# Optimization experiments

Measured on AMD Instinct MI355X. Metric: run time of the kernel, lower is better.

The kernel has to match this reference:

```python
import jax, jax.numpy as jnp
import numpy as np

NL, DM, DS, DC, EX = 4, 1024, 16, 4, 2
DI = EX * DM          # 2048 inner dim
DTR = DM // 16        # 64 dt_rank
HID, OUT = 2048, 1000
B, L = 2, 1024
EPS = 1e-5

def _ln(x, w, b):
    m = jnp.mean(x, -1, keepdims=True)
    v = jnp.var(x, -1, keepdims=True)
    return (x - m) / jnp.sqrt(v + EPS) * w + b

def _silu(x):
    return x * jax.nn.sigmoid(x)

def _dwconv(x, w, b):
    # x: (B,L,C), w: (C,K) depthwise causal conv
    K = w.shape[1]
    xp = jnp.pad(x, ((0, 0), (K - 1, 0), (0, 0)))
    kern = jnp.transpose(w)[:, None, :]  # (K,1,C)
    y = jax.lax.conv_general_dilated(xp, kern, (1,), 'VALID',
                                     dimension_numbers=('NLC', 'LIO', 'NLC'),
                                     feature_group_count=x.shape[-1])
    return y + b

def _selective_scan(xs_, dt, Bm, Cm, A, Dv):
    # xs_, dt: (B,L,DI); Bm, Cm: (B,L,DS); A: (DI,DS); Dv: (DI,)
    def step(h, inp):
        x_t, dt_t, B_t, C_t = inp  # (B,DI),(B,DI),(B,DS),(B,DS)
        dA = jnp.exp(dt_t[..., None] * A)                       # (B,DI,DS)
        h = dA * h + dt_t[..., None] * B_t[:, None, :] * x_t[..., None]
        return h, jnp.einsum('bdn,bn->bd', h, C_t)
    h0 = jnp.zeros((xs_.shape[0], A.shape[0], A.shape[1]), xs_.dtype)
    seq = tuple(jnp.swapaxes(t, 0, 1) for t in (xs_, dt, Bm, Cm))
    _, ys = jax.lax.scan(step, h0, seq)
    return jnp.swapaxes(ys, 0, 1) + xs_ * Dv

def _mamba_block(x, ipw, cw, cb, xpw, dpw, dpb, Alog, Dv, opw):
    xz = jnp.einsum('bld,ed->ble', x, ipw)          # (B,L,2*DI)
    xs_, z = jnp.split(xz, 2, -1)
    xs_ = _silu(_dwconv(xs_, cw, cb))
    xdbl = jnp.einsum('bld,ed->ble', xs_, xpw)      # (B,L,DTR+2*DS)
    dt, Bm, Cm = jnp.split(xdbl, [DTR, DTR + DS], -1)
    dt = jax.nn.softplus(jnp.einsum('blr,dr->bld', dt, dpw) + dpb)
    A = -jnp.exp(Alog)
    y = _selective_scan(xs_, dt, Bm, Cm, A, Dv)
    y = y * _silu(z)
    return jnp.einsum('bld,ed->ble', y, opw)

def setup_inputs() -> dict:
    key = jax.random.key(0)
    ks = jax.random.split(key, 16)
    s = 0.02
    return {
        'x': jax.random.normal(ks[0], (B, L, DM), jnp.float32),
        'ln_w': jnp.ones((NL, DM)), 'ln_b': jnp.zeros((NL, DM)),
        'in_proj_w': jax.random.normal(ks[1], (NL, 2 * DI, DM)) * s,
        'conv_w': jax.random.normal(ks[2], (NL, DI, DC)) * s,
        'conv_b': jnp.zeros((NL, DI)),
        'x_proj_w': jax.random.normal(ks[3], (NL, DTR + 2 * DS, DI)) * s,
        'dt_proj_w': jax.random.normal(ks[4], (NL, DI, DTR)) * s,
        'dt_proj_b': jax.random.uniform(ks[5], (NL, DI), minval=-4.0, maxval=-2.0),
        'A_log': jnp.log(jnp.broadcast_to(jnp.arange(1, DS + 1, dtype=jnp.float32), (NL, DI, DS)) + 0.0),
        'Dv': jnp.ones((NL, DI)),
        'out_proj_w': jax.random.normal(ks[6], (NL, DM, DI)) * s,
        'fn_w': jnp.ones((DM,)), 'fn_b': jnp.zeros((DM,)),
        'h1_w': jax.random.normal(ks[7], (HID, DM)) * s, 'h1_b': jnp.zeros((HID,)),
        'hln_w': jnp.ones((HID,)), 'hln_b': jnp.zeros((HID,)),
        'h2_w': jax.random.normal(ks[8], (OUT, HID)) * s, 'h2_b': jnp.zeros((OUT,)),
    }

def reference(x, ln_w, ln_b, in_proj_w, conv_w, conv_b, x_proj_w, dt_proj_w,
              dt_proj_b, A_log, Dv, out_proj_w, fn_w, fn_b,
              h1_w, h1_b, hln_w, hln_b, h2_w, h2_b):
    for i in range(NL):
        res = x
        xn = _ln(x, ln_w[i], ln_b[i])
        x = _mamba_block(xn, in_proj_w[i], conv_w[i], conv_b[i], x_proj_w[i],
                         dt_proj_w[i], dt_proj_b[i], A_log[i], Dv[i], out_proj_w[i]) + res
    x = _ln(x, fn_w, fn_b)
    last = x[:, -1, :]                               # (B, DM)
    h = jax.nn.gelu(_ln(last @ h1_w.T + h1_b, hln_w, hln_b), approximate=False)
    return h @ h2_w.T + h2_b                         # (B, OUT)
```

## Files before the change

kernel.cpp:

```cpp
#include <hip/hip_runtime.h>

typedef unsigned short u16;
using short8 = __attribute__((ext_vector_type(8))) short;
using f32x4  = __attribute__((ext_vector_type(4))) float;

#define NLAYER 4
#define DMODEL 1024
#define DSTATE 16
#define DINNER 2048
#define DTRANK 64
#define SEQL   1024
#define NBATCH 2
#define MTOK   2048
#define NCH    64
#define CLEN   16

__device__ __forceinline__ u16 f2bf(float f) {
  union { float f; unsigned int u; } cv; cv.f = f;
  return (u16)((cv.u + 0x7FFFu + ((cv.u >> 16) & 1u)) >> 16);
}
__device__ __forceinline__ float bf2f(u16 v) {
  union { unsigned int u; float f; } cv; cv.u = ((unsigned int)v) << 16; return cv.f;
}

__global__ __launch_bounds__(256) void f32_to_bf16_l(const float* __restrict__ src,
                                                     u16* __restrict__ dst, int nper) {
  int l = blockIdx.y;
  int i4 = (blockIdx.x * 256 + threadIdx.x) * 4;
  if (i4 >= nper) return;
  float4 v = *(const float4*)&src[(size_t)l * nper + i4];
  ushort4 o; o.x = f2bf(v.x); o.y = f2bf(v.y); o.z = f2bf(v.z); o.w = f2bf(v.w);
  *(ushort4*)&dst[(size_t)l * nper + i4] = o;
}

__global__ __launch_bounds__(256) void cvt_pad_xproj_l(const float* __restrict__ src,
                                                       u16* __restrict__ dst) {
  int l = blockIdx.y;
  int i4 = (blockIdx.x * 256 + threadIdx.x) * 4;
  int row = i4 >> 11, col = i4 & 2047;
  float4 v = make_float4(0.f, 0.f, 0.f, 0.f);
  if (row < 96) v = *(const float4*)&src[(size_t)l * 96 * 2048 + row * 2048 + col];
  ushort4 o; o.x = f2bf(v.x); o.y = f2bf(v.y); o.z = f2bf(v.z); o.w = f2bf(v.w);
  *(ushort4*)&dst[(size_t)l * 128 * 2048 + i4] = o;
}

__global__ __launch_bounds__(256) void ln_to_bf16_k(const float* __restrict__ X,
    const float* __restrict__ w, const float* __restrict__ b, u16* __restrict__ out) {
  int row = blockIdx.x, tid = threadIdx.x;
  const float* x = X + (size_t)row * 1024;
  float4 v = ((const float4*)x)[tid];
  float s = v.x + v.y + v.z + v.w;
  float q = v.x*v.x + v.y*v.y + v.z*v.z + v.w*v.w;
  for (int o = 32; o; o >>= 1) { s += __shfl_down(s, o); q += __shfl_down(q, o); }
  __shared__ float sb[4], qb[4];
  int wv = tid >> 6, lane = tid & 63;
  if (lane == 0) { sb[wv] = s; qb[wv] = q; }
  __syncthreads();
  s = sb[0] + sb[1] + sb[2] + sb[3];
  q = qb[0] + qb[1] + qb[2] + qb[3];
  float mean = s * (1.f / 1024.f);
  float var  = q * (1.f / 1024.f) - mean * mean;
  float rstd = rsqrtf(var + 1e-5f);
  float4 wv4 = ((const float4*)w)[tid];
  float4 bv4 = ((const float4*)b)[tid];
  ushort4 o4;
  o4.x = f2bf((v.x - mean) * rstd * wv4.x + bv4.x);
  o4.y = f2bf((v.y - mean) * rstd * wv4.y + bv4.y);
  o4.z = f2bf((v.z - mean) * rstd * wv4.z + bv4.z);
  o4.w = f2bf((v.w - mean) * rstd * wv4.w + bv4.w);
  ((ushort4*)(out + (size_t)row * 1024))[tid] = o4;
}

__device__ __forceinline__ void stage_tile(const u16* G, int ld, int row0, int k0,
                                           u16* S, int tid) {
  int w = tid >> 6;
#pragma unroll
  for (int j = 0; j < 2; ++j) {
    int t = tid + j * 256;
    int r = t >> 2;
    int c = (t & 3) << 3;
    const u16* g = G + (size_t)(row0 + r) * ld + (k0 + c);
    u16* s = S + w * 512 + j * 2048;
    __builtin_amdgcn_global_load_lds((const __attribute__((address_space(1))) void*)g,
                                     (__attribute__((address_space(3))) void*)s,
                                     16, 0, 0);
  }
}

template<int EPI, int SWZ>
__global__ __launch_bounds__(256) void gemm_bt(const u16* __restrict__ A,
    const u16* __restrict__ Bw, float* __restrict__ C,
    int lda, int ldb, int ldc, int kchunk, int nbm) {
  __shared__ u16 As[2][128 * 32];
  __shared__ u16 Bs[2][128 * 32];
  int tid = threadIdx.x;
  int bm, bn;
  if (SWZ) {
    int l = blockIdx.x;
    int xcd = l & 7;
    int idx = l >> 3;
    int bnr = (int)(gridDim.x >> 3) / nbm;
    bm = idx % nbm;
    bn = xcd * bnr + idx / nbm;
  } else {
    bm = blockIdx.x; bn = blockIdx.y;
  }
  int kb = blockIdx.z * kchunk, ke = kb + kchunk;
  int lane = tid & 63, w = tid >> 6;
  int wr = (w >> 1) * 64, wc = (w & 1) * 64;
  int fr = lane & 15;
  int kg = (lane >> 4) * 8;
  f32x4 acc[4][4] = {};
  int cur = 0;
  stage_tile(A, lda, bm * 128, kb, As[0], tid);
  stage_tile(Bw, ldb, bn * 128, kb, Bs[0], tid);
  __syncthreads();
  for (int k0 = kb; k0 < ke; k0 += 32) {
    int kn = k0 + 32;
    if (kn < ke) {
      stage_tile(A, lda, bm * 128, kn, As[cur ^ 1], tid);
      stage_tile(Bw, ldb, bn * 128, kn, Bs[cur ^ 1], tid);
    }
    short8 a[4], b[4];
#pragma unroll
    for (int mf = 0; mf < 4; ++mf)
      a[mf] = *(const short8*)&As[cur][(wr + mf * 16 + fr) * 32 + kg];
#pragma unroll
    for (int nf = 0; nf < 4; ++nf)
      b[nf] = *(const short8*)&Bs[cur][(wc + nf * 16 + fr) * 32 + kg];
#pragma unroll
    for (int mf = 0; mf < 4; ++mf)
#pragma unroll
      for (int nf = 0; nf < 4; ++nf)
        acc[mf][nf] = __builtin_amdgcn_mfma_f32_16x16x32_bf16(a[mf], b[nf], acc[mf][nf], 0, 0, 0);
    __syncthreads();
    cur ^= 1;
  }
  int r0 = bm * 128 + wr + (lane >> 4) * 4;
  int c0 = bn * 128 + wc + fr;
#pragma unroll
  for (int mf = 0; mf < 4; ++mf) {
#pragma unroll
    for (int nf = 0; nf < 4; ++nf) {
#pragma unroll
      for (int r = 0; r < 4; ++r) {
        int gr = r0 + mf * 16 + r;
        int gc = c0 + nf * 16;
        float v = acc[mf][nf][r];
        size_t idx = (size_t)gr * ldc + gc;
        if (EPI == 1) {
          ((u16*)C)[idx] = f2bf(v);
        } else {
          atomicAdd(&C[idx], v);
        }
      }
    }
  }
}

__global__ __launch_bounds__(256) void conv_silu_k(const u16* __restrict__ xzb,
    const float* __restrict__ cw, const float* __restrict__ cb,
    u16* __restrict__ xsb) {
  int idx = blockIdx.x * 256 + threadIdx.x;
  int m = idx >> 8;
  int d = (idx & 255) << 3;
  int t = m & (SEQL - 1);
  float4 w4[8];
#pragma unroll
  for (int i = 0; i < 8; ++i) w4[i] = *(const float4*)&cw[(d + i) * 4];
  float acc[8];
#pragma unroll
  for (int q = 0; q < 2; ++q) {
    float4 c4 = *(const float4*)&cb[d + q * 4];
    acc[q*4+0] = c4.x; acc[q*4+1] = c4.y; acc[q*4+2] = c4.z; acc[q*4+3] = c4.w;
  }
#pragma unroll
  for (int j = 0; j < 4; ++j) {
    int tt = t - 3 + j;
    if (tt >= 0) {
      short8 xv = *(const short8*)&xzb[(size_t)(m - 3 + j) * 4096 + d];
#pragma unroll
      for (int i = 0; i < 8; ++i)
        acc[i] += bf2f((u16)xv[i]) * ((const float*)&w4[i])[j];
    }
  }
  short8 ob;
#pragma unroll
  for (int i = 0; i < 8; ++i) {
    float o = acc[i] / (1.f + __expf(-acc[i]));
    ob[i] = (short)f2bf(o);
  }
  *(short8*)&xsb[(size_t)m * 2048 + d] = ob;
}

__global__ __launch_bounds__(256) void gemm_dt_k(const float* __restrict__ Af,
    const u16* __restrict__ Bw, const float* __restrict__ bias, u16* __restrict__ Cout) {
  __shared__ u16 As[128 * 32];
  __shared__ u16 Bs[128 * 32];
  int tid = threadIdx.x;
  int bm = blockIdx.x, bn = blockIdx.y;
  int lane = tid & 63, w = tid >> 6;
  int wr = (w >> 1) * 64, wc = (w & 1) * 64;
  int fr = lane & 15;
  int kg = (lane >> 4) * 8;
  f32x4 acc[4][4] = {};
  int r  = tid >> 1;
  int cc = (tid & 1) * 16;
  for (int k0 = 0; k0 < 64; k0 += 32) {
    const float* src = &Af[(size_t)(bm * 128 + r) * 128 + k0 + cc];
    float4 f0 = *(const float4*)&src[0];
    float4 f1 = *(const float4*)&src[4];
    float4 f2 = *(const float4*)&src[8];
    float4 f3 = *(const float4*)&src[12];
    short8 o0, o1;
    o0[0]=(short)f2bf(f0.x); o0[1]=(short)f2bf(f0.y); o0[2]=(short)f2bf(f0.z); o0[3]=(short)f2bf(f0.w);
    o0[4]=(short)f2bf(f1.x); o0[5]=(short)f2bf(f1.y); o0[6]=(short)f2bf(f1.z); o0[7]=(short)f2bf(f1.w);
    o1[0]=(short)f2bf(f2.x); o1[1]=(short)f2bf(f2.y); o1[2]=(short)f2bf(f2.z); o1[3]=(short)f2bf(f2.w);
    o1[4]=(short)f2bf(f3.x); o1[5]=(short)f2bf(f3.y); o1[6]=(short)f2bf(f3.z); o1[7]=(short)f2bf(f3.w);
    __syncthreads();
    *(short8*)&As[r * 32 + cc]     = o0;
    *(short8*)&As[r * 32 + cc + 8] = o1;
    stage_tile(Bw, 64, bn * 128, k0, Bs, tid);
    __syncthreads();
    short8 a[4], b[4];
#pragma unroll
    for (int mf = 0; mf < 4; ++mf)
      a[mf] = *(const short8*)&As[(wr + mf * 16 + fr) * 32 + kg];
#pragma unroll
    for (int nf = 0; nf < 4; ++nf)
      b[nf] = *(const short8*)&Bs[(wc + nf * 16 + fr) * 32 + kg];
#pragma unroll
    for (int mf = 0; mf < 4; ++mf)
#pragma unroll
      for (int nf = 0; nf < 4; ++nf)
        acc[mf][nf] = __builtin_amdgcn_mfma_f32_16x16x32_bf16(a[mf], b[nf], acc[mf][nf], 0, 0, 0);
  }
  int r0 = bm * 128 + wr + (lane >> 4) * 4;
  int c0 = bn * 128 + wc + fr;
#pragma unroll
  for (int mf = 0; mf < 4; ++mf)
#pragma unroll
    for (int nf = 0; nf < 4; ++nf)
#pragma unroll
      for (int rr = 0; rr < 4; ++rr) {
        int gr = r0 + bm * 0 + mf * 16 + rr;
        int gc = c0 + nf * 16;
        float v = acc[mf][nf][rr] + bias[gc];
        v = (v > 20.f) ? v : log1pf(__expf(v));
        Cout[(size_t)gr * 2048 + gc] = f2bf(v);
      }
}

__global__ __launch_bounds__(256) void scan_part1(const u16* __restrict__ dtb,
    const u16* __restrict__ xsb, const float* __restrict__ xdbl,
    const float* __restrict__ Alog, float* __restrict__ PS_S, float* __restrict__ sumdt_a) {
  int tid = threadIdx.x;
  int dg = blockIdx.x & 7;
  int ch = (blockIdx.x >> 3) & (NCH - 1);
  int b  = blockIdx.x >> 9;
  int d  = dg * 256 + tid;
  float Ar[16];
#pragma unroll
  for (int q = 0; q < 4; ++q) {
    float4 a = *(const float4*)&Alog[d * 16 + q * 4];
    Ar[q*4+0] = -__expf(a.x); Ar[q*4+1] = -__expf(a.y);
    Ar[q*4+2] = -__expf(a.z); Ar[q*4+3] = -__expf(a.w);
  }
  __shared__ float Bsh[CLEN][16];
  {
    int t = tid >> 4, n = tid & 15;
    int mm = b * SEQL + ch * CLEN + t;
    Bsh[t][n] = xdbl[mm * 128 + 64 + n];
  }
  __syncthreads();
  int mbase = b * SEQL + ch * CLEN;
  float dtv[CLEN], xv[CLEN];
#pragma unroll
  for (int t = 0; t < CLEN; ++t) dtv[t] = bf2f(dtb[(size_t)(mbase + t) * 2048 + d]);
#pragma unroll
  for (int t = 0; t < CLEN; ++t) xv[t] = bf2f(xsb[(size_t)(mbase + t) * 2048 + d]);
  float S[16];
#pragma unroll
  for (int n = 0; n < 16; ++n) S[n] = 0.f;
  float sumdt = 0.f;
  for (int t = 0; t < CLEN; ++t) {
    sumdt += dtv[t];
    float dx = dtv[t] * xv[t];
    float4 B0 = *(const float4*)&Bsh[t][0];
    float4 B1 = *(const float4*)&Bsh[t][4];
    float4 B2 = *(const float4*)&Bsh[t][8];
    float4 B3 = *(const float4*)&Bsh[t][12];
    const float* Bp[4] = {(const float*)&B0, (const float*)&B1, (const float*)&B2, (const float*)&B3};
#pragma unroll
    for (int n = 0; n < 16; ++n)
      S[n] = __expf(dtv[t] * Ar[n]) * S[n] + dx * Bp[n >> 2][n & 3];
  }
  size_t base = ((size_t)(b * NCH + ch) * 16) * 2048 + d;
#pragma unroll
  for (int n = 0; n < 16; ++n) PS_S[base + (size_t)n * 2048] = S[n];
  sumdt_a[(size_t)(b * NCH + ch) * 2048 + d] = sumdt;
}

__global__ __launch_bounds__(256) void scan_prefix(const float* __restrict__ PS_S,
    const float* __restrict__ sumdt_a, const float* __restrict__ Alog,
    u16* __restrict__ Hb) {
  int id = blockIdx.x * 256 + threadIdx.x;
  int d = id & 2047;
  int n = (id >> 11) & 15;
  int b = id >> 15;
  float Ar = -__expf(Alog[d * 16 + n]);
  size_t sbase = ((size_t)(b * NCH) * 16 + n) * 2048 + d;
  size_t dbase = (size_t)(b * NCH) * 2048 + d;
  float h = 0.f;
#pragma unroll 8
  for (int ch = 0; ch < NCH; ++ch) {
    Hb[sbase + (size_t)ch * (16 * 2048)] = f2bf(h);
    float S  = PS_S[sbase + (size_t)ch * (16 * 2048)];
    float sd = sumdt_a[dbase + (size_t)ch * 2048];
    h = fmaf(__expf(Ar * sd), h, S);
  }
}

__global__ __launch_bounds__(256) void scan_part2(const u16* __restrict__ dtb,
    const u16* __restrict__ xsb, const float* __restrict__ xdbl,
    const float* __restrict__ Alog, const float* __restrict__ Dv,
    const u16* __restrict__ xzb, const u16* __restrict__ Hb,
    u16* __restrict__ yg) {
  int tid = threadIdx.x;
  int dg = blockIdx.x & 7;
  int ch = (blockIdx.x >> 3) & (NCH - 1);
  int b  = blockIdx.x >> 9;
  int d  = dg * 256 + tid;
  float Ar[16];
#pragma unroll
  for (int q = 0; q < 4; ++q) {
    float4 a = *(const float4*)&Alog[d * 16 + q * 4];
    Ar[q*4+0] = -__expf(a.x); Ar[q*4+1] = -__expf(a.y);
    Ar[q*4+2] = -__expf(a.z); Ar[q*4+3] = -__expf(a.w);
  }
  float Dvd = Dv[d];
  __shared__ float BCs[CLEN][32];
  {
    int t = tid >> 5, n = tid & 31;
    int mm = b * SEQL + ch * CLEN + t;
    BCs[t][n] = xdbl[mm * 128 + 64 + n];
    BCs[t + 8][n] = xdbl[(mm + 8) * 128 + 64 + n];
  }
  size_t hbase = ((size_t)(b * NCH + ch) * 16) * 2048 + d;
  float h[16];
#pragma unroll
  for (int n = 0; n < 16; ++n) h[n] = bf2f(Hb[hbase + (size_t)n * 2048]);
  int mbase = b * SEQL + ch * CLEN;
  float dtv[CLEN], xv[CLEN], zv[CLEN];
#pragma unroll
  for (int t = 0; t < CLEN; ++t) dtv[t] = bf2f(dtb[(size_t)(mbase + t) * 2048 + d]);
#pragma unroll
  for (int t = 0; t < CLEN; ++t) xv[t] = bf2f(xsb[(size_t)(mbase + t) * 2048 + d]);
#pragma unroll
  for (int t = 0; t < CLEN; ++t) zv[t] = bf2f(xzb[(size_t)(mbase + t) * 4096 + 2048 + d]);
  __syncthreads();
  for (int t = 0; t < CLEN; ++t) {
    float dx = dtv[t] * xv[t];
    float4 B0 = *(const float4*)&BCs[t][0];
    float4 B1 = *(const float4*)&BCs[t][4];
    float4 B2 = *(const float4*)&BCs[t][8];
    float4 B3 = *(const float4*)&BCs[t][12];
    float4 C0 = *(const float4*)&BCs[t][16];
    float4 C1 = *(const float4*)&BCs[t][20];
    float4 C2 = *(const float4*)&BCs[t][24];
    float4 C3 = *(const float4*)&BCs[t][28];
    const float* Bp[4] = {(const float*)&B0, (const float*)&B1, (const float*)&B2, (const float*)&B3};
    const float* Cp[4] = {(const float*)&C0, (const float*)&C1, (const float*)&C2, (const float*)&C3};
#pragma unroll
    for (int n = 0; n < 16; ++n)
      h[n] = __expf(dtv[t] * Ar[n]) * h[n] + dx * Bp[n >> 2][n & 3];
    float y0 = 0.f, y1 = 0.f, y2 = 0.f, y3 = 0.f;
#pragma unroll
    for (int n = 0; n < 4; ++n) {
      y0 += h[n]      * Cp[0][n];
      y1 += h[4 + n]  * Cp[1][n];
      y2 += h[8 + n]  * Cp[2][n];
      y3 += h[12 + n] * Cp[3][n];
    }
    float y = (y0 + y1) + (y2 + y3) + xv[t] * Dvd;
    float sz = zv[t] / (1.f + __expf(-zv[t]));
    yg[(size_t)(mbase + t) * 2048 + d] = f2bf(y * sz);
  }
}

__global__ __launch_bounds__(256) void lnlast_gemv1_k(const float* __restrict__ xb,
    const float* __restrict__ fnw, const float* __restrict__ fnb,
    const float* __restrict__ h1w, const float* __restrict__ h1b,
    float* __restrict__ hpre) {
  int blk = blockIdx.x, tid = threadIdx.x;
  int b = blk >> 9;
  int jbase = (blk & 511) * 4;
  int wv = tid >> 6, lane = tid & 63;
  const float* x = xb + (size_t)(b * 1024 + 1023) * 1024;
  float4 v = ((const float4*)x)[tid];
  float s = v.x + v.y + v.z + v.w;
  float q = v.x*v.x + v.y*v.y + v.z*v.z + v.w*v.w;
  for (int o = 32; o; o >>= 1) { s += __shfl_down(s, o); q += __shfl_down(q, o); }
  __shared__ float sb[4], qb[4];
  __shared__ float row[1024];
  if (lane == 0) { sb[wv] = s; qb[wv] = q; }
  __syncthreads();
  s = sb[0] + sb[1] + sb[2] + sb[3];
  q = qb[0] + qb[1] + qb[2] + qb[3];
  float mean = s * (1.f / 1024.f);
  float rstd = rsqrtf(q * (1.f / 1024.f) - mean * mean + 1e-5f);
  float4 wv4 = ((const float4*)fnw)[tid];
  float4 bv4 = ((const float4*)fnb)[tid];
  float4 o;
  o.x = (v.x - mean) * rstd * wv4.x + bv4.x;
  o.y = (v.y - mean) * rstd * wv4.y + bv4.y;
  o.z = (v.z - mean) * rstd * wv4.z + bv4.z;
  o.w = (v.w - mean) * rstd * wv4.w + bv4.w;
  ((float4*)row)[tid] = o;
  __syncthreads();
  int j = jbase + wv;
  const float* w = h1w + (size_t)j * 1024;
  float acc = 0.f;
#pragma unroll
  for (int qq = 0; qq < 4; ++qq) {
    int col = qq * 256 + lane * 4;
    float4 xv = *(const float4*)&row[col];
    float4 wvv = *(const float4*)&w[col];
    acc += xv.x*wvv.x + xv.y*wvv.y + xv.z*wvv.z + xv.w*wvv.w;
  }
  for (int o2 = 32; o2; o2 >>= 1) acc += __shfl_down(acc, o2);
  if (lane == 0) hpre[b * 2048 + j] = acc + h1b[j];
}

__global__ __launch_bounds__(256) void lngelu_gemv2_k(const float* __restrict__ hpre,
    const float* __restrict__ hlnw, const float* __restrict__ hlnb,
    const float* __restrict__ h2w, const float* __restrict__ h2b,
    float* __restrict__ out) {
  int blk = blockIdx.x, tid = threadIdx.x;
  int b = (blk >= 250) ? 1 : 0;
  int jbase = (blk - b * 250) * 4;
  int wv = tid >> 6, lane = tid & 63;
  const float* x = hpre + b * 2048;
  float4 v0 = ((const float4*)x)[tid];
  float4 v1 = ((const float4*)x)[tid + 256];
  float s = v0.x+v0.y+v0.z+v0.w + v1.x+v1.y+v1.z+v1.w;
  float q = v0.x*v0.x+v0.y*v0.y+v0.z*v0.z+v0.w*v0.w
          + v1.x*v1.x+v1.y*v1.y+v1.z*v1.z+v1.w*v1.w;
  for (int o = 32; o; o >>= 1) { s += __shfl_down(s, o); q += __shfl_down(q, o); }
  __shared__ float sb[4], qb[4];
  __shared__ float row[2048];
  if (lane == 0) { sb[wv] = s; qb[wv] = q; }
  __syncthreads();
  s = sb[0] + sb[1] + sb[2] + sb[3];
  q = qb[0] + qb[1] + qb[2] + qb[3];
  float mean = s * (1.f / 2048.f);
  float rstd = rsqrtf(q * (1.f / 2048.f) - mean * mean + 1e-5f);
#pragma unroll
  for (int h = 0; h < 2; ++h) {
    float4 v = h ? v1 : v0;
    int c0 = tid * 4 + h * 1024;
    float4 wv4 = *(const float4*)&hlnw[c0];
    float4 bv4 = *(const float4*)&hlnb[c0];
    float4 g;
    g.x = (v.x - mean) * rstd * wv4.x + bv4.x;
    g.y = (v.y - mean) * rstd * wv4.y + bv4.y;
    g.z = (v.z - mean) * rstd * wv4.z + bv4.z;
    g.w = (v.w - mean) * rstd * wv4.w + bv4.w;
    g.x = 0.5f * g.x * (1.f + erff(g.x * 0.70710678f));
    g.y = 0.5f * g.y * (1.f + erff(g.y * 0.70710678f));
    g.z = 0.5f * g.z * (1.f + erff(g.z * 0.70710678f));
    g.w = 0.5f * g.w * (1.f + erff(g.w * 0.70710678f));
    *(float4*)&row[c0] = g;
  }
  __syncthreads();
  int j = jbase + wv;
  const float* w = h2w + (size_t)j * 2048;
  float acc = 0.f;
#pragma unroll
  for (int qq = 0; qq < 8; ++qq) {
    int col = qq * 256 + lane * 4;
    float4 xv = *(const float4*)&row[col];
    float4 wvv = *(const float4*)&w[col];
    acc += xv.x*wvv.x + xv.y*wvv.y + xv.z*wvv.z + xv.w*wvv.w;
  }
  for (int o2 = 32; o2; o2 >>= 1) acc += __shfl_down(acc, o2);
  if (lane == 0) out[b * 1000 + j] = acc + h2b[j];
}

extern "C" void kernel_launch(void* const* d_in, const int* in_sizes, int n_in,
                              void* d_out, int out_size, void* d_ws, size_t ws_size,
                              hipStream_t stream) {
  const float* x_in = (const float*)d_in[0];
  const float* lnw  = (const float*)d_in[1];
  const float* lnb  = (const float*)d_in[2];
  const float* ipw  = (const float*)d_in[3];
  const float* cw   = (const float*)d_in[4];
  const float* cb   = (const float*)d_in[5];
  const float* xpw  = (const float*)d_in[6];
  const float* dpw  = (const float*)d_in[7];
  const float* dpb  = (const float*)d_in[8];
  const float* Alog = (const float*)d_in[9];
  const float* Dv   = (const float*)d_in[10];
  const float* opw  = (const float*)d_in[11];
  const float* fnw  = (const float*)d_in[12];
  const float* fnb  = (const float*)d_in[13];
  const float* h1w  = (const float*)d_in[14];
  const float* h1b  = (const float*)d_in[15];
  const float* hlnw = (const float*)d_in[16];
  const float* hlnb = (const float*)d_in[17];
  const float* h2w  = (const float*)d_in[18];
  const float* h2b  = (const float*)d_in[19];
  float* out = (float*)d_out;

  char* ws = (char*)d_ws;
  size_t off = 0;
  auto alloc = [&](size_t bytes) -> void* {
    void* p = ws + off; off += (bytes + 255) & ~(size_t)255; return p;
  };
  float* x_buf   = (float*)alloc((size_t)MTOK * DMODEL * 4);
  u16*   xn_bf   = (u16*)  alloc((size_t)MTOK * DMODEL * 2);
  u16*   xz_bf   = (u16*)  alloc((size_t)MTOK * 2 * DINNER * 2);
  u16*   xs_bf   = (u16*)  alloc((size_t)MTOK * DINNER * 2);
  float* xdbl4   = (float*)alloc((size_t)NLAYER * MTOK * 128 * 4);
  u16*   dtb     = (u16*)  alloc((size_t)MTOK * DINNER * 2);
  u16*   yg_bf   = (u16*)  alloc((size_t)MTOK * DINNER * 2);
  u16*   w_ip4   = (u16*)  alloc((size_t)NLAYER * 2 * DINNER * DMODEL * 2);
  u16*   w_xp4   = (u16*)  alloc((size_t)NLAYER * 128 * DINNER * 2);
  u16*   w_dt4   = (u16*)  alloc((size_t)NLAYER * DINNER * DTRANK * 2);
  u16*   w_op4   = (u16*)  alloc((size_t)NLAYER * DMODEL * DINNER * 2);
  float* PS_S    = (float*)alloc((size_t)NBATCH * NCH * 16 * 2048 * 4);
  float* sumdt_a = (float*)alloc((size_t)NBATCH * NCH * 2048 * 4);
  u16*   Hb      = (u16*)  alloc((size_t)NBATCH * NCH * 16 * 2048 * 2);
  float* hpre    = (float*)alloc(2 * 2048 * 4);

  hipMemcpyAsync(x_buf, x_in, (size_t)MTOK * DMODEL * 4, hipMemcpyDeviceToDevice, stream);
  { dim3 g(4096, 4); f32_to_bf16_l<<<g, 256, 0, stream>>>(ipw, w_ip4, 2 * DINNER * DMODEL); }
  { dim3 g(256, 4);  cvt_pad_xproj_l<<<g, 256, 0, stream>>>(xpw, w_xp4); }
  { dim3 g(128, 4);  f32_to_bf16_l<<<g, 256, 0, stream>>>(dpw, w_dt4, DINNER * DTRANK); }
  { dim3 g(2048, 4); f32_to_bf16_l<<<g, 256, 0, stream>>>(opw, w_op4, DMODEL * DINNER); }
  hipMemsetAsync(xdbl4, 0, (size_t)NLAYER * MTOK * 128 * 4, stream);

  for (int i = 0; i < NLAYER; ++i) {
    float* xdbl_l = xdbl4 + (size_t)i * MTOK * 128;
    ln_to_bf16_k<<<MTOK, 256, 0, stream>>>(x_buf, lnw + i * DMODEL, lnb + i * DMODEL, xn_bf);
    gemm_bt<1, 1><<<dim3(512, 1, 1), 256, 0, stream>>>(
        xn_bf, w_ip4 + (size_t)i * 2 * DINNER * DMODEL, (float*)xz_bf,
        1024, 1024, 4096, 1024, 16);
    conv_silu_k<<<2048, 256, 0, stream>>>(xz_bf, cw + (size_t)i * DINNER * 4, cb + i * DINNER, xs_bf);
    { dim3 g(16, 1, 16);
      gemm_bt<3, 0><<<g, 256, 0, stream>>>(xs_bf, w_xp4 + (size_t)i * 128 * DINNER,
                                           xdbl_l, 2048, 2048, 128, 128, 16); }
    { dim3 g(16, 16, 1);
      gemm_dt_k<<<g, 256, 0, stream>>>(xdbl_l, w_dt4 + (size_t)i * DINNER * DTRANK,
                                       dpb + i * DINNER, dtb); }
    scan_part1<<<1024, 256, 0, stream>>>(dtb, xs_bf, xdbl_l,
                                         Alog + (size_t)i * DINNER * DSTATE, PS_S, sumdt_a);
    scan_prefix<<<256, 256, 0, stream>>>(PS_S, sumdt_a, Alog + (size_t)i * DINNER * DSTATE, Hb);
    scan_part2<<<1024, 256, 0, stream>>>(dtb, xs_bf, xdbl_l, Alog + (size_t)i * DINNER * DSTATE,
                                         Dv + i * DINNER, xz_bf, Hb, yg_bf);
    gemm_bt<3, 1><<<dim3(128, 1, 2), 256, 0, stream>>>(
        yg_bf, w_op4 + (size_t)i * DMODEL * DINNER, x_buf,
        2048, 2048, 1024, 1024, 16);
  }
  lnlast_gemv1_k<<<1024, 256, 0, stream>>>(x_buf, fnw, fnb, h1w, h1b, hpre);
  lngelu_gemv2_k<<<500, 256, 0, stream>>>(hpre, hlnw, hlnb, h2w, h2b, out);
  (void)in_sizes; (void)n_in; (void)out_size; (void)ws_size;
}
```

Measured before the change: 750.5 us.

## Widen GEMM blocks to 512 threads and replace x_proj atomics with split-K reduce

The bf16 MFMA GEMM now runs 8 waves per 128x128 tile, each computing a 64x32 sub-tile, and one 16-byte LDS-direct load per thread per operand. The aim is more waves per CU for latency hiding and fewer accumulator registers per thread. The x_proj split-K GEMM now writes per-split partial results to a scratch buffer, and a separate kernel sums the 16 partials. This replaces the fp32 atomicAdd traffic and the up-front memset, at the cost of one extra launch and extra global memory traffic for the partials.

```diff
diff --git a/kernel.cpp b/kernel.cpp
--- a/kernel.cpp
+++ b/kernel.cpp
@@ -14,6 +14,7 @@
 #define MTOK   2048
 #define NCH    64
 #define CLEN   16
+#define XPK    16
 
 __device__ __forceinline__ u16 f2bf(float f) {
   union { float f; unsigned int u; } cv; cv.f = f;
@@ -86,11 +87,21 @@
                                      16, 0, 0);
   }
 }
+__device__ __forceinline__ void stage512(const u16* G, int ld, int row0, int k0,
+                                         u16* S, int tid) {
+  int r = tid >> 2;
+  int c = (tid & 3) << 3;
+  const u16* g = G + (size_t)(row0 + r) * ld + (k0 + c);
+  u16* s = S + (tid >> 6) * 512;
+  __builtin_amdgcn_global_load_lds((const __attribute__((address_space(1))) void*)g,
+                                   (__attribute__((address_space(3))) void*)s,
+                                   16, 0, 0);
+}
 
 template<int EPI, int SWZ>
-__global__ __launch_bounds__(256) void gemm_bt(const u16* __restrict__ A,
+__global__ __launch_bounds__(512) void gemm_bt(const u16* __restrict__ A,
     const u16* __restrict__ Bw, float* __restrict__ C,
-    int lda, int ldb, int ldc, int kchunk, int nbm) {
+    int lda, int ldb, int ldc, int kchunk, int nbm, int zstride) {
   __shared__ u16 As[2][128 * 32];
   __shared__ u16 Bs[2][128 * 32];
   int tid = threadIdx.x;
@@ -106,49 +117,54 @@
     bm = blockIdx.x; bn = blockIdx.y;
   }
   int kb = blockIdx.z * kchunk, ke = kb + kchunk;
-  int lane = tid & 63, w = tid >> 6;
-  int wr = (w >> 1) * 64, wc = (w & 1) * 64;
+  int lane = tid & 63;
+  int w = tid >> 6;
+  int wr = (w >> 2) * 64;
+  int wc = (w & 3) * 32;
   int fr = lane & 15;
   int kg = (lane >> 4) * 8;
-  f32x4 acc[4][4] = {};
+  f32x4 acc[4][2] = {};
   int cur = 0;
-  stage_tile(A, lda, bm * 128, kb, As[0], tid);
-  stage_tile(Bw, ldb, bn * 128, kb, Bs[0], tid);
+  stage512(A, lda, bm * 128, kb, As[0], tid);
+  stage512(Bw, ldb, bn * 128, kb, Bs[0], tid);
   __syncthreads();
   for (int k0 = kb; k0 < ke; k0 += 32) {
     int kn = k0 + 32;
     if (kn < ke) {
-      stage_tile(A, lda, bm * 128, kn, As[cur ^ 1], tid);
-      stage_tile(Bw, ldb, bn * 128, kn, Bs[cur ^ 1], tid);
+      stage512(A, lda, bm * 128, kn, As[cur ^ 1], tid);
+      stage512(Bw, ldb, bn * 128, kn, Bs[cur ^ 1], tid);
     }
-    short8 a[4], b[4];
+    short8 a[4], b[2];
 #pragma unroll
     for (int mf = 0; mf < 4; ++mf)
       a[mf] = *(const short8*)&As[cur][(wr + mf * 16 + fr) * 32 + kg];
 #pragma unroll
-    for (int nf = 0; nf < 4; ++nf)
+    for (int nf = 0; nf < 2; ++nf)
       b[nf] = *(const short8*)&Bs[cur][(wc + nf * 16 + fr) * 32 + kg];
 #pragma unroll
     for (int mf = 0; mf < 4; ++mf)
 #pragma unroll
-      for (int nf = 0; nf < 4; ++nf)
+      for (int nf = 0; nf < 2; ++nf)
         acc[mf][nf] = __builtin_amdgcn_mfma_f32_16x16x32_bf16(a[mf], b[nf], acc[mf][nf], 0, 0, 0);
     __syncthreads();
     cur ^= 1;
   }
   int r0 = bm * 128 + wr + (lane >> 4) * 4;
   int c0 = bn * 128 + wc + fr;
+  size_t zoff = (EPI == 0) ? (size_t)blockIdx.z * zstride : 0;
 #pragma unroll
   for (int mf = 0; mf < 4; ++mf) {
 #pragma unroll
-    for (int nf = 0; nf < 4; ++nf) {
+    for (int nf = 0; nf < 2; ++nf) {
 #pragma unroll
       for (int r = 0; r < 4; ++r) {
         int gr = r0 + mf * 16 + r;
         int gc = c0 + nf * 16;
         float v = acc[mf][nf][r];
         size_t idx = (size_t)gr * ldc + gc;
-        if (EPI == 1) {
+        if (EPI == 0) {
+          C[zoff + idx] = v;
+        } else if (EPI == 1) {
           ((u16*)C)[idx] = f2bf(v);
         } else {
           atomicAdd(&C[idx], v);
@@ -156,6 +172,18 @@
       }
     }
   }
+}
+
+__global__ __launch_bounds__(256) void reduce_xdbl_k(const float* __restrict__ part,
+                                                     float* __restrict__ xdbl_l) {
+  int i4 = (blockIdx.x * 256 + threadIdx.x) * 4;
+  float4 s = *(const float4*)&part[i4];
+#pragma unroll
+  for (int z = 1; z < XPK; ++z) {
+    float4 v = *(const float4*)&part[(size_t)z * (MTOK * 128) + i4];
+    s.x += v.x; s.y += v.y; s.z += v.z; s.w += v.w;
+  }
+  *(float4*)&xdbl_l[i4] = s;
 }
 
 __global__ __launch_bounds__(256) void conv_silu_k(const u16* __restrict__ xzb,
@@ -243,7 +271,7 @@
     for (int nf = 0; nf < 4; ++nf)
 #pragma unroll
       for (int rr = 0; rr < 4; ++rr) {
-        int gr = r0 + bm * 0 + mf * 16 + rr;
+        int gr = r0 + mf * 16 + rr;
         int gc = c0 + nf * 16;
         float v = acc[mf][nf][rr] + bias[gc];
         v = (v > 20.f) ? v : log1pf(__expf(v));
@@ -521,7 +549,8 @@
   u16*   xn_bf   = (u16*)  alloc((size_t)MTOK * DMODEL * 2);
   u16*   xz_bf   = (u16*)  alloc((size_t)MTOK * 2 * DINNER * 2);
   u16*   xs_bf   = (u16*)  alloc((size_t)MTOK * DINNER * 2);
-  float* xdbl4   = (float*)alloc((size_t)NLAYER * MTOK * 128 * 4);
+  float* xpart   = (float*)alloc((size_t)XPK * MTOK * 128 * 4);
+  float* xdbl_l  = (float*)alloc((size_t)MTOK * 128 * 4);
   u16*   dtb     = (u16*)  alloc((size_t)MTOK * DINNER * 2);
   u16*   yg_bf   = (u16*)  alloc((size_t)MTOK * DINNER * 2);
   u16*   w_ip4   = (u16*)  alloc((size_t)NLAYER * 2 * DINNER * DMODEL * 2);
@@ -538,18 +567,17 @@
   { dim3 g(256, 4);  cvt_pad_xproj_l<<<g, 256, 0, stream>>>(xpw, w_xp4); }
   { dim3 g(128, 4);  f32_to_bf16_l<<<g, 256, 0, stream>>>(dpw, w_dt4, DINNER * DTRANK); }
   { dim3 g(2048, 4); f32_to_bf16_l<<<g, 256, 0, stream>>>(opw, w_op4, DMODEL * DINNER); }
-  hipMemsetAsync(xdbl4, 0, (size_t)NLAYER * MTOK * 128 * 4, stream);
 
   for (int i = 0; i < NLAYER; ++i) {
-    float* xdbl_l = xdbl4 + (size_t)i * MTOK * 128;
     ln_to_bf16_k<<<MTOK, 256, 0, stream>>>(x_buf, lnw + i * DMODEL, lnb + i * DMODEL, xn_bf);
-    gemm_bt<1, 1><<<dim3(512, 1, 1), 256, 0, stream>>>(
+    gemm_bt<1, 1><<<dim3(512, 1, 1), 512, 0, stream>>>(
         xn_bf, w_ip4 + (size_t)i * 2 * DINNER * DMODEL, (float*)xz_bf,
-        1024, 1024, 4096, 1024, 16);
+        1024, 1024, 4096, 1024, 16, 0);
     conv_silu_k<<<2048, 256, 0, stream>>>(xz_bf, cw + (size_t)i * DINNER * 4, cb + i * DINNER, xs_bf);
-    { dim3 g(16, 1, 16);
-      gemm_bt<3, 0><<<g, 256, 0, stream>>>(xs_bf, w_xp4 + (size_t)i * 128 * DINNER,
-                                           xdbl_l, 2048, 2048, 128, 128, 16); }
+    { dim3 g(16, 1, XPK);
+      gemm_bt<0, 0><<<g, 512, 0, stream>>>(xs_bf, w_xp4 + (size_t)i * 128 * DINNER,
+                                           xpart, 2048, 2048, 128, 128, 16, MTOK * 128); }
+    reduce_xdbl_k<<<256, 256, 0, stream>>>(xpart, xdbl_l);
     { dim3 g(16, 16, 1);
       gemm_dt_k<<<g, 256, 0, stream>>>(xdbl_l, w_dt4 + (size_t)i * DINNER * DTRANK,
                                        dpb + i * DINNER, dtb); }
@@ -558,9 +586,9 @@
     scan_prefix<<<256, 256, 0, stream>>>(PS_S, sumdt_a, Alog + (size_t)i * DINNER * DSTATE, Hb);
     scan_part2<<<1024, 256, 0, stream>>>(dtb, xs_bf, xdbl_l, Alog + (size_t)i * DINNER * DSTATE,
                                          Dv + i * DINNER, xz_bf, Hb, yg_bf);
-    gemm_bt<3, 1><<<dim3(128, 1, 2), 256, 0, stream>>>(
+    gemm_bt<3, 1><<<dim3(128, 1, 2), 512, 0, stream>>>(
         yg_bf, w_op4 + (size_t)i * DMODEL * DINNER, x_buf,
-        2048, 2048, 1024, 1024, 16);
+        2048, 2048, 1024, 1024, 16, 0);
   }
   lnlast_gemv1_k<<<1024, 256, 0, stream>>>(x_buf, fnw, fnb, h1w, h1b, hpre);
   lngelu_gemv2_k<<<500, 256, 0, stream>>>(hpre, hlnw, hlnb, h2w, h2b, out);
```

Measured after the change: 693.4 us. 7.6% less time.
